# Performance work log

Hardware: AMD Instinct MI355X
Metric: run time of the kernel (lower is better)

## Reference

```python
import jax, jax.numpy as jnp
import numpy as np

EPS = 1e-5
NUM_GRAPHS = 1000


def _glorot(key, shape):
    fan_in, fan_out = shape[1], shape[0]
    lim = float(np.sqrt(6.0 / (fan_in + fan_out)))
    return jax.random.uniform(key, shape, jnp.float32, -lim, lim)


def setup_inputs() -> dict:
    N, E, C, D, L = 100_000, 1_600_000, 10_000, 32, 4
    key = jax.random.key(0)
    ks = jax.random.split(key, 12)
    x = jax.random.normal(ks[0], (N, 2), jnp.float32)
    edge_index = jax.random.randint(ks[1], (2, E), 0, N)
    edge_attr = jax.random.normal(ks[2], (E, 1), jnp.float32)
    candidate_idxs = jax.random.randint(ks[3], (C,), 0, N)
    batch = jnp.sort(jax.random.randint(ks[4], (N,), 0, NUM_GRAPHS))
    lk = jax.random.split(ks[5], L)
    lk2 = jax.random.split(ks[6], L)
    return {
        "x": x,
        "edge_index": edge_index,
        "edge_attr": edge_attr,
        "candidate_idxs": candidate_idxs,
        "batch": batch,
        "lin_in_w": _glorot(ks[7], (D, 2)),
        "lin_in_b": jnp.zeros((D,), jnp.float32),
        "w1": jnp.stack([_glorot(lk[i], (D, 2 * D + 1)) for i in range(L)]),
        "b1": jnp.zeros((L, D), jnp.float32),
        "bn1_g": jnp.ones((L, D), jnp.float32),
        "bn1_b": jnp.zeros((L, D), jnp.float32),
        "w2": jnp.stack([_glorot(lk2[i], (D, D)) for i in range(L)]),
        "b2": jnp.zeros((L, D), jnp.float32),
        "bn2_g": jnp.ones((L, D), jnp.float32),
        "bn2_b": jnp.zeros((L, D), jnp.float32),
        "lin_out_w": _glorot(ks[8], (1, D)),
        "lin_out_b": jnp.zeros((), jnp.float32),
    }


def _batchnorm(m, g, b):
    # training-mode BatchNorm1d over the edge (row) axis, biased variance
    mu = jnp.mean(m, axis=0)
    var = jnp.mean(jnp.square(m - mu), axis=0)
    return (m - mu) * jax.lax.rsqrt(var + EPS) * g + b


def reference(x, edge_index, edge_attr, candidate_idxs, batch,
              lin_in_w, lin_in_b, w1, b1, bn1_g, bn1_b,
              w2, b2, bn2_g, bn2_b, lin_out_w, lin_out_b):
    N = x.shape[0]
    src, dst = edge_index[0], edge_index[1]  # x_j = x[src], x_i = x[dst]
    h = x @ lin_in_w.T + lin_in_b  # [N, D]
    for l in range(w1.shape[0]):
        msg = jnp.concatenate([h[dst], h[src], edge_attr], axis=-1)  # [E, 2D+1]
        m = jax.nn.relu(_batchnorm(msg @ w1[l].T + b1[l], bn1_g[l], bn1_b[l]))
        m = jax.nn.relu(_batchnorm(m @ w2[l].T + b2[l], bn2_g[l], bn2_b[l]))
        h = h + jax.ops.segment_sum(m, dst, num_segments=N)
    logits = (h[candidate_idxs] @ lin_out_w.T)[:, 0] + lin_out_b  # [C]
    seg = batch[candidate_idxs]
    mx = jax.ops.segment_max(logits, seg, num_segments=NUM_GRAPHS)
    mx = jnp.where(jnp.isfinite(mx), mx, 0.0)
    lse = mx + jnp.log(jax.ops.segment_sum(jnp.exp(logits - mx[seg]), seg,
                                           num_segments=NUM_GRAPHS))
    return logits - lse[seg]
```

## Files before the change

kernel.cpp:

```cpp
#include <hip/hip_runtime.h>
#include <stdint.h>

#define NGRAPH 1000

typedef __attribute__((ext_vector_type(8))) short short8;
typedef __attribute__((ext_vector_type(4))) float f32x4;

static __device__ __forceinline__ uint32_t pack2_bf16(float a, float b) {
  uint32_t ua = __float_as_uint(a), ub = __float_as_uint(b);
  ua = (ua + 0x7fffu + ((ua >> 16) & 1u)) >> 16;
  ub = (ub + 0x7fffu + ((ub >> 16) & 1u)) >> 16;
  return ua | (ub << 16);
}
static __device__ __forceinline__ unsigned short f2bf(float x) {
  uint32_t u = __float_as_uint(x);
  u = (u + 0x7fffu + ((u >> 16) & 1u)) >> 16;
  return (unsigned short)u;
}
static __device__ __forceinline__ float bf2f(unsigned short u) {
  return __uint_as_float(((uint32_t)u) << 16);
}
union frag_u { short8 v; uint32_t u[4]; };

__global__ __launch_bounds__(256) void k_prep(const float* __restrict__ w1,
                                              float* __restrict__ w1n,
                                              float* __restrict__ w1c) {
  int t = blockIdx.x * 256 + threadIdx.x;
  if (t < 4 * 2048) {
    int l = t >> 11, r = t & 2047, k = r >> 6, o = r & 63;
    w1n[t] = (o < 32) ? w1[l * 2080 + o * 65 + k]
                      : w1[l * 2080 + (o - 32) * 65 + (k + 32)];
  } else if (t < 4 * 2048 + 4 * 32) {
    int u = t - 4 * 2048;
    int l = u >> 5, d = u & 31;
    w1c[u] = w1[l * 2080 + d * 65 + 64];
  }
}

__global__ __launch_bounds__(256) void k_init(const float* __restrict__ x,
                                              const float* __restrict__ wi,
                                              const float* __restrict__ bi,
                                              float* __restrict__ h, int N) {
  int t = blockIdx.x * 256 + threadIdx.x;
  if (t >= N * 32) return;
  int n = t >> 5, d = t & 31;
  h[t] = fmaf(x[2 * n], wi[2 * d], fmaf(x[2 * n + 1], wi[2 * d + 1], bi[d]));
}

__global__ __launch_bounds__(256) void k_zero32(int* __restrict__ p, int n) {
  int t = blockIdx.x * 256 + threadIdx.x;
  if (t < n) p[t] = 0;
}

#define CHUNK 2048
__global__ __launch_bounds__(256) void k_bucket(const int* __restrict__ src,
                                                const int* __restrict__ dst,
                                                const float* __restrict__ ea,
                                                int* __restrict__ gcur,
                                                int* __restrict__ bsrc,
                                                int* __restrict__ bdst,
                                                float* __restrict__ bea,
                                                int E, int pstep, int cap) {
  __shared__ int lcnt[8], lbase[8];
  const int t = threadIdx.x;
  const int base = blockIdx.x * CHUNK;
  if (t < 8) lcnt[t] = 0;
  __syncthreads();
  int es[8], ds[8], ps[8];
  float eas[8];
#pragma unroll
  for (int j = 0; j < 8; j++) {
    int e = base + j * 256 + t;
    bool ok = e < E;
    int d = ok ? dst[e] : 0;
    es[j] = ok ? src[e] : 0;
    eas[j] = ok ? ea[e] : 0.f;
    ds[j] = d;
    ps[j] = ok ? (d / pstep) : -1;
    if (ok) atomicAdd(&lcnt[ps[j]], 1);
  }
  __syncthreads();
  if (t < 8) lbase[t] = atomicAdd(&gcur[t], lcnt[t]);
  __syncthreads();
  if (t < 8) lcnt[t] = lbase[t];
  __syncthreads();
#pragma unroll
  for (int j = 0; j < 8; j++) {
    if (ps[j] >= 0) {
      int pos = atomicAdd(&lcnt[ps[j]], 1);
      if (pos < cap) {
        int idx = ps[j] * cap + pos;
        bsrc[idx] = es[j];
        bdst[idx] = ds[j];
        bea[idx] = eas[j];
      }
    }
  }
}

__global__ __launch_bounds__(256) void k_hist2(const int* __restrict__ bdst,
                                               const int* __restrict__ gcur,
                                               int* __restrict__ cnt, int cap) {
  const int g = blockIdx.x & 7;
  const int len = gcur[g];
  const int stride = (gridDim.x >> 3) * 256;
  const int* bd = bdst + (size_t)g * cap;
  for (int i = (blockIdx.x >> 3) * 256 + threadIdx.x; i < len; i += stride)
    atomicAdd(cnt + bd[i], 1);
}

__global__ __launch_bounds__(256) void k_scan1(const int* __restrict__ in,
                                               int* __restrict__ out,
                                               int* __restrict__ bsum, int n) {
  __shared__ int sh[256];
  const int t = threadIdx.x;
  const int idx = blockIdx.x * 1024 + t * 4;
  int v[4];
#pragma unroll
  for (int j = 0; j < 4; j++) v[j] = (idx + j < n) ? in[idx + j] : 0;
  int tsum = v[0] + v[1] + v[2] + v[3];
  sh[t] = tsum;
  __syncthreads();
#pragma unroll
  for (int ofs = 1; ofs < 256; ofs <<= 1) {
    int x = (t >= ofs) ? sh[t - ofs] : 0;
    __syncthreads();
    sh[t] += x;
    __syncthreads();
  }
  int run = sh[t] - tsum;
  if (t == 255) bsum[blockIdx.x] = sh[255];
#pragma unroll
  for (int j = 0; j < 4; j++) {
    if (idx + j < n) out[idx + j] = run;
    run += v[j];
  }
}
__global__ __launch_bounds__(256) void k_scan2(int* __restrict__ bsum, int nb) {
  __shared__ int sh[256];
  const int t = threadIdx.x;
  int val = (t < nb) ? bsum[t] : 0;
  sh[t] = val;
  __syncthreads();
#pragma unroll
  for (int ofs = 1; ofs < 256; ofs <<= 1) {
    int x = (t >= ofs) ? sh[t - ofs] : 0;
    __syncthreads();
    sh[t] += x;
    __syncthreads();
  }
  if (t < nb) bsum[t] = sh[t] - val;
}
__global__ __launch_bounds__(256) void k_scan3(int* __restrict__ rowptr,
                                               const int* __restrict__ bsum,
                                               int* __restrict__ cur, int n) {
  int t = blockIdx.x * 256 + threadIdx.x;
  if (t >= n) return;
  int v = rowptr[t] + bsum[t >> 10];
  rowptr[t] = v;
  cur[t] = v;
}

__global__ __launch_bounds__(256) void k_scatter2(const int* __restrict__ bsrc,
                                                  const int* __restrict__ bdst,
                                                  const float* __restrict__ bea,
                                                  const int* __restrict__ gcur,
                                                  int* __restrict__ cur,
                                                  uint2* __restrict__ sedge, int cap) {
  const int g = blockIdx.x & 7;
  const int len = gcur[g];
  const int stride = (gridDim.x >> 3) * 256;
  const size_t o = (size_t)g * cap;
  for (int i = (blockIdx.x >> 3) * 256 + threadIdx.x; i < len; i += stride) {
    int d = bdst[o + i];
    int pos = atomicAdd(cur + d, 1);
    sedge[pos] = make_uint2((unsigned)bsrc[o + i], __float_as_uint(bea[o + i]));
  }
}

__global__ __launch_bounds__(256) void k_fillrid(const int* __restrict__ rowptr,
                                                 const int* __restrict__ cnt,
                                                 int* __restrict__ rid_s, int N) {
  const int n = blockIdx.x * 8 + (threadIdx.x >> 5);
  if (n >= N) return;
  const int j0 = threadIdx.x & 31;
  const int start = rowptr[n], deg = cnt[n];
  for (int j = j0; j < deg; j += 32) rid_s[start + j] = n;
}

__global__ __launch_bounds__(256) void k_node(const float* __restrict__ h,
                                              const float* __restrict__ w1n,
                                              unsigned short* __restrict__ hAB, int N) {
  const int wid = (blockIdx.x * 256 + threadIdx.x) >> 6;
  const int lane = threadIdx.x & 63;
  if (wid >= N) return;
  const int n = __builtin_amdgcn_readfirstlane(wid);
  const float* hn = h + (size_t)n * 32;
  float acc = 0.f;
#pragma unroll
  for (int k = 0; k < 32; k++) acc = fmaf(hn[k], w1n[k * 64 + lane], acc);
  hAB[(size_t)n * 64 + lane] = f2bf(acc);
}

static __device__ __forceinline__ void block_stats_reduce(float* ssum, float* ssq,
                                                          float* __restrict__ stats) {
  __shared__ float red[4][64];
  const int lane = threadIdx.x & 63, wv = threadIdx.x >> 6;
#pragma unroll
  for (int q = 0; q < 32; q++) {
    float a = ssum[q], b = ssq[q];
#pragma unroll
    for (int m = 32; m >= 1; m >>= 1) {
      a += __shfl_xor(a, m, 64);
      b += __shfl_xor(b, m, 64);
    }
    if (lane == 0) { red[wv][q] = a; red[wv][32 + q] = b; }
  }
  __syncthreads();
  if (threadIdx.x < 64) {
    int q = threadIdx.x;
    stats[(size_t)blockIdx.x * 64 + q] = red[0][q] + red[1][q] + red[2][q] + red[3][q];
  }
}

__global__ __launch_bounds__(256, 2) void k_combine(
    const uint32_t* __restrict__ hAB, const uint2* __restrict__ sedge,
    const int* __restrict__ rid_s, const float* __restrict__ w1c,
    uint32_t* __restrict__ mpre, float* __restrict__ stats, int E) {
  float ssum[32], ssq[32];
#pragma unroll
  for (int q = 0; q < 32; q++) { ssum[q] = 0.f; ssq[q] = 0.f; }
  const int stride = gridDim.x * blockDim.x;
  for (int pos = blockIdx.x * blockDim.x + threadIdx.x; pos < E; pos += stride) {
    const uint2 se = sedge[pos];
    const int vs = (int)se.x;
    const float eav = __uint_as_float(se.y);
    const int rid = rid_s[pos];
    const uint4* pa = (const uint4*)(hAB + (size_t)rid * 32);
    const uint4* pb = (const uint4*)(hAB + (size_t)vs * 32 + 16);
    uint4 au[4], bu[4];
#pragma unroll
    for (int q = 0; q < 4; q++) { au[q] = pa[q]; bu[q] = pb[q]; }
    const uint32_t* ad = (const uint32_t*)au;
    const uint32_t* bd = (const uint32_t*)bu;
    float m[32];
#pragma unroll
    for (int p = 0; p < 16; p++) {
      float a0 = __uint_as_float(ad[p] << 16), a1 = __uint_as_float(ad[p] & 0xffff0000u);
      float b0 = __uint_as_float(bd[p] << 16), b1 = __uint_as_float(bd[p] & 0xffff0000u);
      m[2 * p]     = a0 + fmaf(eav, w1c[2 * p],     b0);
      m[2 * p + 1] = a1 + fmaf(eav, w1c[2 * p + 1], b1);
    }
    uint4* mp = (uint4*)(mpre + (size_t)pos * 16);
    mp[0] = make_uint4(pack2_bf16(m[0], m[1]), pack2_bf16(m[2], m[3]),
                       pack2_bf16(m[4], m[5]), pack2_bf16(m[6], m[7]));
    mp[1] = make_uint4(pack2_bf16(m[8], m[9]), pack2_bf16(m[10], m[11]),
                       pack2_bf16(m[12], m[13]), pack2_bf16(m[14], m[15]));
    mp[2] = make_uint4(pack2_bf16(m[16], m[17]), pack2_bf16(m[18], m[19]),
                       pack2_bf16(m[20], m[21]), pack2_bf16(m[22], m[23]));
    mp[3] = make_uint4(pack2_bf16(m[24], m[25]), pack2_bf16(m[26], m[27]),
                       pack2_bf16(m[28], m[29]), pack2_bf16(m[30], m[31]));
#pragma unroll
    for (int q = 0; q < 32; q++) { ssum[q] += m[q]; ssq[q] = fmaf(m[q], m[q], ssq[q]); }
  }
  block_stats_reduce(ssum, ssq, stats);
}

__global__ __launch_bounds__(256) void k_finalize(const float* __restrict__ stats, int nblk, int E,
                                                  const float* __restrict__ g,
                                                  const float* __restrict__ bb,
                                                  float* __restrict__ ss) {
  const int q = blockIdx.x;
  const int t = threadIdx.x;
  double s0 = 0.0, s1 = 0.0;
  for (int i = t; i < nblk; i += 256) {
    s0 += (double)stats[(size_t)i * 64 + q];
    s1 += (double)stats[(size_t)i * 64 + 32 + q];
  }
  __shared__ double r0[256], r1[256];
  r0[t] = s0; r1[t] = s1;
  __syncthreads();
#pragma unroll
  for (int m = 128; m >= 1; m >>= 1) {
    if (t < m) { r0[t] += r0[t + m]; r1[t] += r1[t + m]; }
    __syncthreads();
  }
  if (t == 0) {
    double invE = 1.0 / (double)E;
    double mu = r0[0] * invE;
    double var = r1[0] * invE - mu * mu;
    if (var < 0.0) var = 0.0;
    double sc = (double)g[q] / sqrt(var + 1e-5);
    ss[q] = (float)sc;
    ss[32 + q] = (float)((double)bb[q] - mu * sc);
  }
}

__global__ __launch_bounds__(256) void k_gemm2m(
    uint32_t* __restrict__ mpre, const float* __restrict__ ss,
    const float* __restrict__ w2, float* __restrict__ stats, int E) {
  const int lane = threadIdx.x & 63;
  const int wv = threadIdx.x >> 6;
  const int row = lane & 15;
  const int kb = (lane >> 4) * 8;
  const int G = E >> 4;
  const int gstart = blockIdx.x * 4 + wv;
  const int gstride = gridDim.x * 4;

  float sc[8], sh[8];
#pragma unroll
  for (int j = 0; j < 8; j++) { sc[j] = ss[kb + j]; sh[j] = ss[32 + kb + j]; }

  frag_u b0, b1;
#pragma unroll
  for (int p = 0; p < 4; p++) {
    const float* wp0 = w2 + (size_t)row * 32 + kb + 2 * p;
    const float* wp1 = w2 + (size_t)(row + 16) * 32 + kb + 2 * p;
    b0.u[p] = pack2_bf16(wp0[0], wp0[1]);
    b1.u[p] = pack2_bf16(wp1[0], wp1[1]);
  }

  float sum0 = 0.f, sq0 = 0.f, sum1 = 0.f, sq1 = 0.f;
  unsigned short* mp16 = (unsigned short*)mpre;

  for (int g = gstart; g < G; g += gstride) {
    const int e0 = g << 4;
    const uint4 raw = *(const uint4*)(mpre + (size_t)(e0 + row) * 16 + (lane >> 4) * 4);
    float m[8];
    m[0] = __uint_as_float(raw.x << 16); m[1] = __uint_as_float(raw.x & 0xffff0000u);
    m[2] = __uint_as_float(raw.y << 16); m[3] = __uint_as_float(raw.y & 0xffff0000u);
    m[4] = __uint_as_float(raw.z << 16); m[5] = __uint_as_float(raw.z & 0xffff0000u);
    m[6] = __uint_as_float(raw.w << 16); m[7] = __uint_as_float(raw.w & 0xffff0000u);
    frag_u a;
#pragma unroll
    for (int p = 0; p < 4; p++) {
      float x0 = fmaxf(fmaf(m[2 * p],     sc[2 * p],     sh[2 * p]),     0.f);
      float x1 = fmaxf(fmaf(m[2 * p + 1], sc[2 * p + 1], sh[2 * p + 1]), 0.f);
      a.u[p] = pack2_bf16(x0, x1);
    }
    f32x4 z = {0.f, 0.f, 0.f, 0.f};
    f32x4 acc0 = __builtin_amdgcn_mfma_f32_16x16x32_bf16(a.v, b0.v, z, 0, 0, 0);
    f32x4 acc1 = __builtin_amdgcn_mfma_f32_16x16x32_bf16(a.v, b1.v, z, 0, 0, 0);
#pragma unroll
    for (int r = 0; r < 4; r++) {
      sum0 += acc0[r]; sq0 = fmaf(acc0[r], acc0[r], sq0);
      sum1 += acc1[r]; sq1 = fmaf(acc1[r], acc1[r], sq1);
      const size_t base = (size_t)(e0 + (lane >> 4) * 4 + r) * 32;
      mp16[base + row]      = f2bf(acc0[r]);
      mp16[base + row + 16] = f2bf(acc1[r]);
    }
  }

  sum0 += __shfl_xor(sum0, 16); sum0 += __shfl_xor(sum0, 32);
  sq0  += __shfl_xor(sq0, 16);  sq0  += __shfl_xor(sq0, 32);
  sum1 += __shfl_xor(sum1, 16); sum1 += __shfl_xor(sum1, 32);
  sq1  += __shfl_xor(sq1, 16);  sq1  += __shfl_xor(sq1, 32);
  __shared__ float red[4][64];
  if (lane < 16) {
    red[wv][row] = sum0;      red[wv][16 + row] = sum1;
    red[wv][32 + row] = sq0;  red[wv][48 + row] = sq1;
  }
  __syncthreads();
  if (threadIdx.x < 64) {
    int q = threadIdx.x;
    stats[(size_t)blockIdx.x * 64 + q] = red[0][q] + red[1][q] + red[2][q] + red[3][q];
  }
}

__global__ __launch_bounds__(256) void k_agg(
    const unsigned short* __restrict__ mp16, const int* __restrict__ rowptr,
    const int* __restrict__ cnt, const float* __restrict__ ss,
    float* __restrict__ h, int N) {
  const int n = blockIdx.x * 8 + (threadIdx.x >> 5);
  if (n >= N) return;
  const int d = threadIdx.x & 31;
  const int start = rowptr[n];
  const int deg = cnt[n];
  const float sc = ss[d], sh = ss[32 + d];
  const unsigned short* p = mp16 + (size_t)start * 32 + d;
  float acc = 0.f;
  int j = 0;
  for (; j + 2 <= deg; j += 2) {
    float x0 = bf2f(p[(size_t)j * 32]);
    float x1 = bf2f(p[(size_t)(j + 1) * 32]);
    acc += fmaxf(fmaf(x0, sc, sh), 0.f);
    acc += fmaxf(fmaf(x1, sc, sh), 0.f);
  }
  if (j < deg) {
    float x0 = bf2f(p[(size_t)j * 32]);
    acc += fmaxf(fmaf(x0, sc, sh), 0.f);
  }
  h[(size_t)n * 32 + d] += acc;
}

__global__ __launch_bounds__(256) void k_initseg(unsigned* __restrict__ segmax,
                                                 float* __restrict__ segsum) {
  int t = blockIdx.x * 256 + threadIdx.x;
  if (t < NGRAPH) { segmax[t] = 0u; segsum[t] = 0.f; }
}

__global__ __launch_bounds__(256) void k_logits(
    const float* __restrict__ h, const int* __restrict__ cand, const int* __restrict__ batch,
    const float* __restrict__ wout, const float* __restrict__ bout,
    float* __restrict__ logits, int* __restrict__ seg, unsigned* __restrict__ segmax, int C) {
  int t = blockIdx.x * 256 + threadIdx.x;
  if (t >= C) return;
  int node = cand[t];
  const float4* hp = (const float4*)(h + (size_t)node * 32);
  float acc = bout[0];
#pragma unroll
  for (int kc = 0; kc < 8; kc++) {
    float4 v = hp[kc];
    acc = fmaf(v.x, wout[kc * 4 + 0], acc);
    acc = fmaf(v.y, wout[kc * 4 + 1], acc);
    acc = fmaf(v.z, wout[kc * 4 + 2], acc);
    acc = fmaf(v.w, wout[kc * 4 + 3], acc);
  }
  logits[t] = acc;
  int s = batch[node];
  seg[t] = s;
  unsigned o = __float_as_uint(acc);
  o ^= (o >> 31) ? 0xFFFFFFFFu : 0x80000000u;
  atomicMax(segmax + s, o);
}

static __device__ __forceinline__ float o2f(unsigned o) {
  o ^= (o & 0x80000000u) ? 0x80000000u : 0xFFFFFFFFu;
  return __uint_as_float(o);
}

__global__ __launch_bounds__(256) void k_expsum(const float* __restrict__ logits,
                                                const int* __restrict__ seg,
                                                const unsigned* __restrict__ segmax,
                                                float* __restrict__ segsum, int C) {
  int t = blockIdx.x * 256 + threadIdx.x;
  if (t >= C) return;
  int s = seg[t];
  float mx = o2f(segmax[s]);
  atomicAdd(segsum + s, expf(logits[t] - mx));
}

__global__ __launch_bounds__(256) void k_out(const float* __restrict__ logits,
                                             const int* __restrict__ seg,
                                             const unsigned* __restrict__ segmax,
                                             const float* __restrict__ segsum,
                                             float* __restrict__ out, int C) {
  int t = blockIdx.x * 256 + threadIdx.x;
  if (t >= C) return;
  int s = seg[t];
  out[t] = logits[t] - (o2f(segmax[s]) + logf(segsum[s]));
}

extern "C" void kernel_launch(void* const* d_in, const int* in_sizes, int n_in,
                              void* d_out, int out_size, void* d_ws, size_t ws_size,
                              hipStream_t stream) {
  const float* x     = (const float*)d_in[0];
  const int*   eidx  = (const int*)d_in[1];
  const float* eattr = (const float*)d_in[2];
  const int*   cand  = (const int*)d_in[3];
  const int*   batch = (const int*)d_in[4];
  const float* wi    = (const float*)d_in[5];
  const float* bi    = (const float*)d_in[6];
  const float* w1    = (const float*)d_in[7];
  const float* g1    = (const float*)d_in[9];
  const float* bb1   = (const float*)d_in[10];
  const float* w2    = (const float*)d_in[11];
  const float* g2    = (const float*)d_in[13];
  const float* bb2   = (const float*)d_in[14];
  const float* wout  = (const float*)d_in[15];
  const float* bout  = (const float*)d_in[16];

  const int N = in_sizes[4];
  const int E = in_sizes[2];
  const int C = in_sizes[3];
  const int* src  = eidx;
  const int* dstp = eidx + E;

  char* ws = (char*)d_ws;
  size_t off = 0;
  auto carve = [&](size_t bytes) {
    void* p = ws + off;
    off = (off + bytes + 255) & ~(size_t)255;
    return p;
  };
  const int NBLK = 1024;
  uint32_t* mpre   = (uint32_t*)carve((size_t)E * 64);
  float*    h      = (float*)carve((size_t)N * 32 * 4);
  uint32_t* hAB    = (uint32_t*)carve((size_t)N * 128);
  float*    w1n    = (float*)carve(4 * 2048 * 4);
  float*    w1c    = (float*)carve(4 * 32 * 4);
  float*    ss     = (float*)carve(64 * 4);
  float*    stats  = (float*)carve((size_t)NBLK * 64 * 4);
  int*      cnt    = (int*)carve((size_t)N * 4);
  int*      rowptr = (int*)carve((size_t)N * 4);
  int*      cur    = (int*)carve((size_t)N * 4);
  int*      bsum   = (int*)carve(256 * 4);
  uint2*    sedge  = (uint2*)carve((size_t)E * 8);
  int*      rid_s  = (int*)carve((size_t)E * 4);
  int*      gcur   = (int*)carve(8 * 4);
  float*    logits = (float*)carve((size_t)C * 4);
  int*      seg    = (int*)carve((size_t)C * 4);
  unsigned* segmax = (unsigned*)carve(NGRAPH * 4);
  float*    segsum = (float*)carve(NGRAPH * 4);
  (void)ws_size; (void)n_in; (void)out_size;

  const int cap = E / 8 + 65536;
  int*   bsrc = (int*)mpre;
  int*   bdst = bsrc + (size_t)8 * cap;
  float* bea  = (float*)(bdst + (size_t)8 * cap);

  const int nb1 = (N + 1023) / 1024;
  const int pstep = (N + 7) / 8;
  k_zero32<<<(N + 255) / 256, 256, 0, stream>>>(cnt, N);
  k_zero32<<<1, 256, 0, stream>>>(gcur, 8);
  k_bucket<<<(E + CHUNK - 1) / CHUNK, 256, 0, stream>>>(src, dstp, eattr, gcur,
                                                        bsrc, bdst, bea, E, pstep, cap);
  k_hist2<<<1024, 256, 0, stream>>>(bdst, gcur, cnt, cap);
  k_scan1<<<nb1, 256, 0, stream>>>(cnt, rowptr, bsum, N);
  k_scan2<<<1, 256, 0, stream>>>(bsum, nb1);
  k_scan3<<<(N + 255) / 256, 256, 0, stream>>>(rowptr, bsum, cur, N);
  k_scatter2<<<1024, 256, 0, stream>>>(bsrc, bdst, bea, gcur, cur, sedge, cap);
  k_fillrid<<<(N + 7) / 8, 256, 0, stream>>>(rowptr, cnt, rid_s, N);

  k_prep<<<33, 256, 0, stream>>>(w1, w1n, w1c);
  k_init<<<(N * 32 + 255) / 256, 256, 0, stream>>>(x, wi, bi, h, N);

  for (int l = 0; l < 4; l++) {
    k_node<<<(N * 64 + 255) / 256, 256, 0, stream>>>(h, w1n + l * 2048,
                                                     (unsigned short*)hAB, N);
    k_combine<<<NBLK, 256, 0, stream>>>(hAB, sedge, rid_s, w1c + l * 32,
                                        mpre, stats, E);
    k_finalize<<<32, 256, 0, stream>>>(stats, NBLK, E, g1 + l * 32, bb1 + l * 32, ss);
    k_gemm2m<<<NBLK, 256, 0, stream>>>(mpre, ss, w2 + l * 1024, stats, E);
    k_finalize<<<32, 256, 0, stream>>>(stats, NBLK, E, g2 + l * 32, bb2 + l * 32, ss);
    k_agg<<<(N + 7) / 8, 256, 0, stream>>>((const unsigned short*)mpre, rowptr, cnt,
                                           ss, h, N);
  }

  k_initseg<<<(NGRAPH + 255) / 256, 256, 0, stream>>>(segmax, segsum);
  k_logits<<<(C + 255) / 256, 256, 0, stream>>>(h, cand, batch, wout, bout,
                                                logits, seg, segmax, C);
  k_expsum<<<(C + 255) / 256, 256, 0, stream>>>(logits, seg, segmax, segsum, C);
  k_out<<<(C + 255) / 256, 256, 0, stream>>>(logits, seg, segmax, segsum, (float*)d_out, C);
}
```

Before: 852.3 us.

## Route histogram and scatter work to XCD-local buckets via dynamic chunk claiming

The histogram and scatter kernels now read the hardware XCD id from a register and start work on the dst-partitioned bucket that matches their own XCD. Blocks claim chunks of that bucket through an atomic work counter, then move on to the other buckets in turn. Before, the bucket was fixed by blockIdx. The aim is to keep atomics on cnt/cur inside the local XCD's L2 slice to cut cross-die coherence traffic, and to balance load dynamically. In exchange it adds per-chunk global atomics and barriers, and it relies on the hardware register encoding being correct.

```diff
diff --git a/kernel.cpp b/kernel.cpp
--- a/kernel.cpp
+++ b/kernel.cpp
@@ -21,6 +21,10 @@
   return __uint_as_float(((uint32_t)u) << 16);
 }
 union frag_u { short8 v; uint32_t u[4]; };
+
+static __device__ __forceinline__ int my_xcd() {
+  return __builtin_amdgcn_s_getreg(63508) & 7;
+}
 
 __global__ __launch_bounds__(256) void k_prep(const float* __restrict__ w1,
                                               float* __restrict__ w1n,
@@ -98,15 +102,28 @@
   }
 }
 
+#define CLAIM 2048
 __global__ __launch_bounds__(256) void k_hist2(const int* __restrict__ bdst,
                                                const int* __restrict__ gcur,
-                                               int* __restrict__ cnt, int cap) {
-  const int g = blockIdx.x & 7;
-  const int len = gcur[g];
-  const int stride = (gridDim.x >> 3) * 256;
-  const int* bd = bdst + (size_t)g * cap;
-  for (int i = (blockIdx.x >> 3) * 256 + threadIdx.x; i < len; i += stride)
-    atomicAdd(cnt + bd[i], 1);
+                                               int* __restrict__ cnt, int cap,
+                                               int* __restrict__ pcur) {
+  __shared__ int base_sh;
+  const int xcc = my_xcd();
+  for (int gi = 0; gi < 8; gi++) {
+    const int g = (xcc + gi) & 7;
+    const int len = gcur[g];
+    const int* bd = bdst + (size_t)g * cap;
+    while (true) {
+      if (threadIdx.x == 0) base_sh = atomicAdd(&pcur[g], CLAIM);
+      __syncthreads();
+      const int base = base_sh;
+      __syncthreads();
+      if (base >= len) break;
+      const int end = min(base + CLAIM, len);
+      for (int i = base + threadIdx.x; i < end; i += 256)
+        atomicAdd(cnt + bd[i], 1);
+    }
+  }
 }
 
 __global__ __launch_bounds__(256) void k_scan1(const int* __restrict__ in,
@@ -166,15 +183,27 @@
                                                   const float* __restrict__ bea,
                                                   const int* __restrict__ gcur,
                                                   int* __restrict__ cur,
-                                                  uint2* __restrict__ sedge, int cap) {
-  const int g = blockIdx.x & 7;
-  const int len = gcur[g];
-  const int stride = (gridDim.x >> 3) * 256;
-  const size_t o = (size_t)g * cap;
-  for (int i = (blockIdx.x >> 3) * 256 + threadIdx.x; i < len; i += stride) {
-    int d = bdst[o + i];
-    int pos = atomicAdd(cur + d, 1);
-    sedge[pos] = make_uint2((unsigned)bsrc[o + i], __float_as_uint(bea[o + i]));
+                                                  uint2* __restrict__ sedge, int cap,
+                                                  int* __restrict__ pcur) {
+  __shared__ int base_sh;
+  const int xcc = my_xcd();
+  for (int gi = 0; gi < 8; gi++) {
+    const int g = (xcc + gi) & 7;
+    const int len = gcur[g];
+    const size_t o = (size_t)g * cap;
+    while (true) {
+      if (threadIdx.x == 0) base_sh = atomicAdd(&pcur[g], CLAIM);
+      __syncthreads();
+      const int base = base_sh;
+      __syncthreads();
+      if (base >= len) break;
+      const int end = min(base + CLAIM, len);
+      for (int i = base + threadIdx.x; i < end; i += 256) {
+        int d = bdst[o + i];
+        int pos = atomicAdd(cur + d, 1);
+        sedge[pos] = make_uint2((unsigned)bsrc[o + i], __float_as_uint(bea[o + i]));
+      }
+    }
   }
 }
 
@@ -497,13 +526,16 @@
   int*      bsum   = (int*)carve(256 * 4);
   uint2*    sedge  = (uint2*)carve((size_t)E * 8);
   int*      rid_s  = (int*)carve((size_t)E * 4);
-  int*      gcur   = (int*)carve(8 * 4);
+  int*      gcur   = (int*)carve(24 * 4);
   float*    logits = (float*)carve((size_t)C * 4);
   int*      seg    = (int*)carve((size_t)C * 4);
   unsigned* segmax = (unsigned*)carve(NGRAPH * 4);
   float*    segsum = (float*)carve(NGRAPH * 4);
   (void)ws_size; (void)n_in; (void)out_size;
 
+  int* pcurA = gcur + 8;
+  int* pcurB = gcur + 16;
+
   const int cap = E / 8 + 65536;
   int*   bsrc = (int*)mpre;
   int*   bdst = bsrc + (size_t)8 * cap;
@@ -512,14 +544,14 @@
   const int nb1 = (N + 1023) / 1024;
   const int pstep = (N + 7) / 8;
   k_zero32<<<(N + 255) / 256, 256, 0, stream>>>(cnt, N);
-  k_zero32<<<1, 256, 0, stream>>>(gcur, 8);
+  k_zero32<<<1, 256, 0, stream>>>(gcur, 24);
   k_bucket<<<(E + CHUNK - 1) / CHUNK, 256, 0, stream>>>(src, dstp, eattr, gcur,
                                                         bsrc, bdst, bea, E, pstep, cap);
-  k_hist2<<<1024, 256, 0, stream>>>(bdst, gcur, cnt, cap);
+  k_hist2<<<1024, 256, 0, stream>>>(bdst, gcur, cnt, cap, pcurA);
   k_scan1<<<nb1, 256, 0, stream>>>(cnt, rowptr, bsum, N);
   k_scan2<<<1, 256, 0, stream>>>(bsum, nb1);
   k_scan3<<<(N + 255) / 256, 256, 0, stream>>>(rowptr, bsum, cur, N);
-  k_scatter2<<<1024, 256, 0, stream>>>(bsrc, bdst, bea, gcur, cur, sedge, cap);
+  k_scatter2<<<1024, 256, 0, stream>>>(bsrc, bdst, bea, gcur, cur, sedge, cap, pcurB);
   k_fillrid<<<(N + 7) / 8, 256, 0, stream>>>(rowptr, cnt, rid_s, N);
 
   k_prep<<<33, 256, 0, stream>>>(w1, w1n, w1c);
```

After: 994.6 us. +16.7%, slower.
